# Kernel optimization log

Hardware: AMD Instinct MI355X
Metric: run time of the kernel (lower is better)

The kernel has to match this reference:

```python
import jax, jax.numpy as jnp
import numpy as np
from jax import lax

BS = 16; NG = 512; L = 2048; HOP = 512; ZD = 128; HD = 512
FS = L // 2 + 1
TAR = (NG - 1) * HOP + L  # 263680, matches int((NG+3)/4*L)
PPC = 5; PPK = 65
LOG10 = float(np.log(10.0))

def _hann_periodic(n):
    return (0.5 * (1.0 - np.cos(2.0 * np.pi * np.arange(n) / n))).astype(np.float32)

# filter window: fftshift(hann_window(L)) (torch periodic hann)
_FW = jnp.asarray(np.fft.fftshift(_hann_periodic(L)))
# OLA windows with edge correction (first/last grain half set to center value 1.0)
_w = _hann_periodic(L)
_ow = np.tile(_w[None, :], (NG, 1))
_ow[0, : L // 2] = _w[L // 2]
_ow[-1, L // 2 :] = _w[L // 2]
_OLA_W = jnp.asarray(_ow)  # [NG, L]
# overlap-add scatter indices and divisor (fold(unfold(ones)))
_IDX = jnp.asarray((np.arange(NG)[:, None] * HOP + np.arange(L)[None, :]).reshape(-1))
_DIV = jnp.zeros((TAR,), jnp.float32).at[_IDX].add(1.0)


def setup_inputs() -> dict:
    key = jax.random.key(0)
    ks = jax.random.split(key, 8)
    s = 0.02
    d = {}
    d["z"] = jax.random.normal(ks[0], (BS * NG, ZD), jnp.float32)
    d["w0"] = jax.random.normal(ks[1], (ZD, HD), jnp.float32) * s
    d["b0"] = jnp.zeros((HD,), jnp.float32)
    d["g0"] = jnp.ones((HD,), jnp.float32)
    d["be0"] = jnp.zeros((HD,), jnp.float32)
    d["w1"] = jax.random.normal(ks[2], (HD, HD), jnp.float32) * s
    d["b1"] = jnp.zeros((HD,), jnp.float32)
    d["g1"] = jnp.ones((HD,), jnp.float32)
    d["be1"] = jnp.zeros((HD,), jnp.float32)
    d["w2"] = jax.random.normal(ks[3], (HD, HD), jnp.float32) * s
    d["b2"] = jnp.zeros((HD,), jnp.float32)
    d["g2"] = jnp.ones((HD,), jnp.float32)
    d["be2"] = jnp.zeros((HD,), jnp.float32)
    d["w3"] = jax.random.normal(ks[4], (HD, FS), jnp.float32) * s
    d["b3"] = jnp.zeros((FS,), jnp.float32)
    d["pp_w"] = jax.random.normal(ks[5], (1, PPC, PPK), jnp.float32) * s
    d["pp_b"] = jnp.zeros((1,), jnp.float32)
    d["noise"] = jax.random.uniform(ks[6], (BS * NG, L), jnp.float32) * 2.0 - 1.0
    return d


def _lin_bn_lrelu(x, w, b, g, be):
    h = x @ w + b
    m = h.mean(0)
    v = jnp.mean((h - m) ** 2, 0)  # biased var (train-mode BatchNorm1d)
    h = (h - m) * lax.rsqrt(v + 1e-5) * g + be
    return jnp.where(h >= 0, h, 0.2 * h)  # LeakyReLU(0.2)


def reference(z, w0, b0, g0, be0, w1, b1, g1, be1, w2, b2, g2, be2, w3, b3, pp_w, pp_b, noise):
    # decoder MLP -> filter coefficients
    h = _lin_bn_lrelu(z, w0, b0, g0, be0)
    h = _lin_bn_lrelu(h, w1, b1, g1, be1)
    h = _lin_bn_lrelu(h, w2, b2, g2, be2)
    fc = h @ w3 + b3  # [BS*NG, FS]
    fc = 2.0 * jax.nn.sigmoid(fc) ** LOG10 + 1e-7  # mod_sigmoid
    # noise filtering in spectral domain
    ir = jnp.fft.irfft(fc.astype(jnp.complex64), n=L, axis=-1).astype(jnp.float32)
    ir = jnp.fft.fftshift(ir * _FW[None, :], axes=-1)
    audio = jnp.fft.irfft(jnp.fft.rfft(noise, axis=-1) * jnp.fft.rfft(ir, axis=-1), n=L, axis=-1).astype(jnp.float32)
    # per-grain windowing + overlap-add (nn.Fold equivalent scatter-add)
    audio = audio.reshape(BS, NG, L) * _OLA_W[None]
    audio_sum = jnp.zeros((BS, TAR), jnp.float32).at[:, _IDX].add(audio.reshape(BS, -1))
    audio_sum = audio_sum / _DIV  # normalize_ola
    # post-processing conv (PPC replicated channels -> 1) + softsign
    x = jnp.broadcast_to(audio_sum[:, None, :], (BS, PPC, TAR))
    y = lax.conv_general_dilated(x, pp_w, (1,), [(PPK // 2, PPK // 2)], dimension_numbers=("NCH", "OIH", "NCH"))
    y = y[:, 0, :] + pp_b[0]
    return y / (1.0 + jnp.abs(y))
```

## Files before the change

kernel.cpp:

```cpp
#include <hip/hip_runtime.h>
#include <hip/hip_bf16.h>
#include <math.h>

#define TARLEN 263680
#define POWEXP 2.302585092994046f
#define PC(i) ((i) + ((i) >> 3))

typedef __attribute__((ext_vector_type(8))) short bf16x8;
typedef __attribute__((ext_vector_type(8))) ushort u16x8;
typedef __attribute__((ext_vector_type(4))) float f32x4;

__device__ __forceinline__ void gload16(const void* g, void* l) {
    __builtin_amdgcn_global_load_lds((const __attribute__((address_space(1))) void*)g,
                                     (__attribute__((address_space(3))) void*)l, 16, 0, 0);
}

__device__ __forceinline__ float bf16f(ushort u) {
    union { uint u; float f; } v; v.u = (uint)u << 16; return v.f;
}
__device__ __forceinline__ ushort fbf16(float x) {
    __hip_bfloat16 h = __float2bfloat16(x);
    return *reinterpret_cast<ushort*>(&h);
}

__device__ __forceinline__ float vsin_rev(float rev) {
    float r; asm("v_sin_f32 %0, %1" : "=v"(r) : "v"(rev)); return r;
}
__device__ __forceinline__ float vcos_rev(float rev) {
    float r; asm("v_cos_f32 %0, %1" : "=v"(r) : "v"(rev)); return r;
}

template<int EPI>
__global__ __launch_bounds__(512) void gemm8(
    const ushort* __restrict__ A, const ushort* __restrict__ Bt,
    const float* __restrict__ bias, ushort* __restrict__ C,
    int K, int Nvalid, int ldc,
    float* __restrict__ ps, float* __restrict__ pq)
{
    __shared__ ushort As[3][4096];
    __shared__ ushort Bs[3][4096];
    __shared__ float sred[8][2][16];
    __shared__ float qred[8][2][16];
    const int tid = threadIdx.x;
    const int lane = tid & 63;
    const int wid = tid >> 6;
    const int nwg = gridDim.x * gridDim.y;
    const int bid = blockIdx.y * gridDim.x + blockIdx.x;
    const int q8 = nwg >> 3;
    const int swzb = (bid & 7) * q8 + (bid >> 3);
    const int bx = swzb % gridDim.x;
    const int by = swzb / gridDim.x;
    const int m0 = by * 128;
    const int n0 = bx * 128;
    const int NT = K >> 5;

    f32x4 acc[4][2];
#pragma unroll
    for (int m = 0; m < 4; ++m)
#pragma unroll
        for (int n = 0; n < 2; ++n)
            acc[m][n] = (f32x4){0.f, 0.f, 0.f, 0.f};

    const int srow = tid >> 2;
    const int scol = (((tid & 3) ^ ((tid >> 3) & 3)) << 3);

    auto stage = [&](int t, int buf) {
        const int k0 = t << 5;
        gload16(A + (size_t)(m0 + srow) * K + k0 + scol, &As[buf][tid * 8]);
        gload16(Bt + (size_t)(n0 + srow) * K + k0 + scol, &Bs[buf][tid * 8]);
    };

    const int lr = lane & 15;
    const int sw8 = (((lane >> 4) ^ ((lane >> 1) & 3)) << 3);
    const int wm0 = (wid >> 2) * 64;
    const int wn0 = (wid & 3) * 32;

    stage(0, 0);
    stage(1, 1);
    for (int t = 0; t < NT; ++t) {
        const int cur = t % 3;
        if (t + 2 < NT) {
            asm volatile("s_waitcnt vmcnt(2)" ::: "memory");
            __builtin_amdgcn_s_barrier();
            stage(t + 2, (t + 2) % 3);
        } else {
            asm volatile("s_waitcnt vmcnt(0)" ::: "memory");
            __builtin_amdgcn_s_barrier();
        }
        const ushort* as = As[cur];
        const ushort* bs = Bs[cur];
        bf16x8 af[4], bfv[2];
#pragma unroll
        for (int m = 0; m < 4; ++m)
            af[m] = *reinterpret_cast<const bf16x8*>(&as[(wm0 + m * 16 + lr) * 32 + sw8]);
#pragma unroll
        for (int n = 0; n < 2; ++n)
            bfv[n] = *reinterpret_cast<const bf16x8*>(&bs[(wn0 + n * 16 + lr) * 32 + sw8]);
#pragma unroll
        for (int m = 0; m < 4; ++m)
#pragma unroll
            for (int n = 0; n < 2; ++n)
                acc[m][n] = __builtin_amdgcn_mfma_f32_16x16x32_bf16(af[m], bfv[n], acc[m][n], 0, 0, 0);
    }
    __syncthreads();

    const int cr = (lane >> 4) << 2;
    const int cc = lane & 15;
    float sacc[2] = {0.f, 0.f}, qacc[2] = {0.f, 0.f};
#pragma unroll
    for (int m = 0; m < 4; ++m) {
#pragma unroll
        for (int n = 0; n < 2; ++n) {
            int gcol = n0 + wn0 + n * 16 + cc;
            if (EPI == 0 || gcol < Nvalid) {
                float bv = bias[gcol];
                int grow = m0 + wm0 + m * 16 + cr;
#pragma unroll
                for (int j = 0; j < 4; ++j) {
                    float v = acc[m][n][j] + bv;
                    if (EPI == 1) {
                        float sg = 1.f / (1.f + __expf(-v));
                        v = 2.f * __expf(POWEXP * __logf(sg)) + 1e-7f;
                    } else {
                        sacc[n] += v;
                        qacc[n] += v * v;
                    }
                    C[(size_t)(grow + j) * ldc + gcol] = fbf16(v);
                }
            }
        }
    }
    if (EPI == 0) {
#pragma unroll
        for (int n = 0; n < 2; ++n) {
            float s = sacc[n], q = qacc[n];
            s += __shfl_xor(s, 16); q += __shfl_xor(q, 16);
            s += __shfl_xor(s, 32); q += __shfl_xor(q, 32);
            if (lane < 16) { sred[wid][n][lane] = s; qred[wid][n][lane] = q; }
        }
        __syncthreads();
        if (tid < 128) {
            int wn_ = tid >> 5, n_ = (tid >> 4) & 1, cc_ = tid & 15;
            float s = sred[wn_][n_][cc_] + sred[4 + wn_][n_][cc_];
            float q = qred[wn_][n_][cc_] + qred[4 + wn_][n_][cc_];
            int col = n0 + wn_ * 32 + n_ * 16 + cc_;
            ps[(size_t)by * 512 + col] = s;
            pq[(size_t)by * 512 + col] = q;
        }
    }
}

__global__ __launch_bounds__(256) void prep_stats_act_k(
    const ushort* __restrict__ Hb, const float* __restrict__ ps,
    const float* __restrict__ pq, const float* __restrict__ gamma,
    const float* __restrict__ beta, ushort* __restrict__ A)
{
    __shared__ float sa[512], sb[512];
    const int tid = threadIdx.x;
    for (int c = tid; c < 512; c += 256) {
        float s = 0.f, q = 0.f;
#pragma unroll 8
        for (int rg = 0; rg < 64; ++rg) { s += ps[rg * 512 + c]; q += pq[rg * 512 + c]; }
        float m = s * (1.f / 8192.f);
        float v = q * (1.f / 8192.f) - m * m;
        float rs = rsqrtf(v + 1e-5f);
        float a = rs * gamma[c];
        sa[c] = a;
        sb[c] = beta[c] - m * a;
    }
    __syncthreads();
    const int col0 = (tid * 8) & 511;
    float ra[8], rb[8];
#pragma unroll
    for (int j = 0; j < 8; ++j) { ra[j] = sa[col0 + j]; rb[j] = sb[col0 + j]; }
    size_t base = (size_t)blockIdx.x * 16384;
#pragma unroll
    for (int it = 0; it < 8; ++it) {
        int off = (it * 256 + tid) << 3;
        u16x8 hv = *reinterpret_cast<const u16x8*>(&Hb[base + off]);
        u16x8 o;
#pragma unroll
        for (int j = 0; j < 8; ++j) {
            float y = fmaf(bf16f(hv[j]), ra[j], rb[j]);
            o[j] = fbf16(y >= 0.f ? y : 0.2f * y);
        }
        *reinterpret_cast<u16x8*>(&A[base + off]) = o;
    }
}

__global__ __launch_bounds__(256) void prep_inputs(
    const float* __restrict__ w0, const float* __restrict__ w1,
    const float* __restrict__ w2, const float* __restrict__ w3,
    const float* __restrict__ z,
    ushort* __restrict__ B0, ushort* __restrict__ B1,
    ushort* __restrict__ B2, ushort* __restrict__ B3,
    ushort* __restrict__ A)
{
    if (blockIdx.z == 4) {
        int bid = blockIdx.y * gridDim.x + blockIdx.x;
        if (bid >= 512) return;
        int idx = (bid * 256 + threadIdx.x) << 3;
        float4 a = *reinterpret_cast<const float4*>(&z[idx]);
        float4 b = *reinterpret_cast<const float4*>(&z[idx + 4]);
        float x[8] = {a.x, a.y, a.z, a.w, b.x, b.y, b.z, b.w};
        u16x8 o;
#pragma unroll
        for (int j = 0; j < 8; ++j) o[j] = fbf16(x[j]);
        *reinterpret_cast<u16x8*>(&A[idx]) = o;
        return;
    }
    const float* w; ushort* Bt; int K, N, GX, GY;
    switch (blockIdx.z) {
        case 0: w = w0; Bt = B0; K = 128; N = 512;  GX = 4;  GY = 16; break;
        case 1: w = w1; Bt = B1; K = 512; N = 512;  GX = 16; GY = 16; break;
        case 2: w = w2; Bt = B2; K = 512; N = 512;  GX = 16; GY = 16; break;
        default:w = w3; Bt = B3; K = 512; N = 1025; GX = 16; GY = 36; break;
    }
    if ((int)blockIdx.x >= GX || (int)blockIdx.y >= GY) return;
    __shared__ float tile[32][33];
    int k0 = blockIdx.x * 32, n0 = blockIdx.y * 32;
    int tx = threadIdx.x & 31, ty = threadIdx.x >> 5;
#pragma unroll
    for (int r = 0; r < 4; ++r) {
        int k = k0 + ty + r * 8;
        int n = n0 + tx;
        tile[ty + r * 8][tx] = (n < N) ? w[(size_t)k * N + n] : 0.f;
    }
    __syncthreads();
#pragma unroll
    for (int r = 0; r < 4; ++r) {
        int n = n0 + ty + r * 8;
        int k = k0 + tx;
        Bt[(size_t)n * K + k] = fbf16(tile[tx][ty + r * 8]);
    }
}

__device__ __forceinline__ float2 cmul(float2 a, float c, float s) {
    return make_float2(a.x * c - a.y * s, a.x * s + a.y * c);
}

template<bool INV, int L>
__device__ __forceinline__ void stk_stage(
    const float2* __restrict__ s, float2* __restrict__ d, int t)
{
    int k = t & (L - 1);
    float2 x0 = s[PC(t)];
    float2 x1 = s[PC(t + 256)];
    float2 x2 = s[PC(t + 512)];
    float2 x3 = s[PC(t + 768)];
    if (L > 1) {
        float rev = (float)k * (1.0f / (float)(4 * L));
        float s1 = vsin_rev(rev), c1 = vcos_rev(rev);
        if (!INV) s1 = -s1;
        float c2 = c1 * c1 - s1 * s1, s2 = 2.f * c1 * s1;
        float c3 = c2 * c1 - s2 * s1, s3 = s2 * c1 + c2 * s1;
        x1 = cmul(x1, c1, s1);
        x2 = cmul(x2, c2, s2);
        x3 = cmul(x3, c3, s3);
    }
    float2 a = make_float2(x0.x + x2.x, x0.y + x2.y);
    float2 b = make_float2(x0.x - x2.x, x0.y - x2.y);
    float2 c = make_float2(x1.x + x3.x, x1.y + x3.y);
    float2 e = make_float2(x1.x - x3.x, x1.y - x3.y);
    int db = ((t - k) << 2) + k;
    d[PC(db)]         = make_float2(a.x + c.x, a.y + c.y);
    d[PC(db + 2 * L)] = make_float2(a.x - c.x, a.y - c.y);
    if (!INV) {
        d[PC(db + L)]     = make_float2(b.x + e.y, b.y - e.x);
        d[PC(db + 3 * L)] = make_float2(b.x - e.y, b.y + e.x);
    } else {
        d[PC(db + L)]     = make_float2(b.x - e.y, b.y + e.x);
        d[PC(db + 3 * L)] = make_float2(b.x + e.y, b.y - e.x);
    }
}

__global__ __launch_bounds__(256) void fft_filter_kernel(
    const float* __restrict__ noise, const ushort* __restrict__ fcsb,
    ushort* __restrict__ awb)
{
    __shared__ float2 X[1152], Y[1152];
    __shared__ ushort Fb[1026];
    const int tid = threadIdx.x;
    const int r = blockIdx.x;

    const float2* nrow = reinterpret_cast<const float2*>(noise + ((size_t)r << 11));
    for (int i = tid; i < 1025; i += 256) Fb[i] = fcsb[(size_t)r * 1040 + i];
    {
        float2 x0 = nrow[tid], x1 = nrow[tid + 256], x2 = nrow[tid + 512], x3 = nrow[tid + 768];
        float2 a = make_float2(x0.x + x2.x, x0.y + x2.y);
        float2 b = make_float2(x0.x - x2.x, x0.y - x2.y);
        float2 c = make_float2(x1.x + x3.x, x1.y + x3.y);
        float2 e = make_float2(x1.x - x3.x, x1.y - x3.y);
        int db = tid << 2;
        Y[PC(db)]     = make_float2(a.x + c.x, a.y + c.y);
        Y[PC(db + 1)] = make_float2(b.x + e.y, b.y - e.x);
        Y[PC(db + 2)] = make_float2(a.x - c.x, a.y - c.y);
        Y[PC(db + 3)] = make_float2(b.x - e.y, b.y + e.x);
    }
    __syncthreads();
    stk_stage<false, 4>(Y, X, tid);   __syncthreads();
    stk_stage<false, 16>(X, Y, tid);  __syncthreads();
    stk_stage<false, 64>(Y, X, tid);  __syncthreads();
    stk_stage<false, 256>(X, Y, tid); __syncthreads();

    const float INV1024 = 1.0f / 1024.0f;
    auto proc = [&](int k, float c, float s) {
        int k2 = (1024 - k) & 1023;
        float2 za = Y[PC(k)], zb = Y[PC(k2)];
        float Fer = 0.5f * (za.x + zb.x), Fei = 0.5f * (za.y - zb.y);
        float For = 0.5f * (za.y + zb.y), Foi = 0.5f * (zb.x - za.x);
        float wFr = c * For - s * Foi;
        float wFi = c * Foi + s * For;
        float Xkr = Fer + wFr, Xki = Fei + wFi;
        float Xbr = Fer - wFr, Xbi = wFi - Fei;
        float Hk, Hb;
        {
            float cl = (k == 0) ? bf16f(Fb[1]) : bf16f(Fb[k - 1]);
            float crr = (k == 1024) ? bf16f(Fb[1023]) : bf16f(Fb[k + 1]);
            float h = 0.5f * bf16f(Fb[k]) + 0.25f * (cl + crr);
            Hk = ((k & 1) ? -h : h) * INV1024;
        }
        {
            int kb = 1024 - k;
            float cl = (kb == 0) ? bf16f(Fb[1]) : bf16f(Fb[kb - 1]);
            float crr = (kb == 1024) ? bf16f(Fb[1023]) : bf16f(Fb[kb + 1]);
            float h = 0.5f * bf16f(Fb[kb]) + 0.25f * (cl + crr);
            Hb = ((kb & 1) ? -h : h) * INV1024;
        }
        float Ykr = Hk * Xkr, Yki = Hk * Xki;
        float Ybr = Hb * Xbr, Ybi = Hb * Xbi;
        if (k == 0) {
            X[PC(0)] = make_float2(0.5f * (Ykr + Ybr), 0.5f * (Ykr - Ybr));
        } else {
            float Ger = 0.5f * (Ykr + Ybr), Gei = 0.5f * (Yki - Ybi);
            float Sgr = 0.5f * (Ykr - Ybr), Sgi = 0.5f * (Yki + Ybi);
            float wpr = c, wpi = -s;
            float Gor = wpr * Sgr - wpi * Sgi;
            float Goi = wpr * Sgi + wpi * Sgr;
            X[PC(k)]  = make_float2(Ger - Goi, Gei + Gor);
            X[PC(k2)] = make_float2(Ger + Goi, Gor - Gei);
        }
    };
    {
        float rev0 = (float)tid * (1.0f / 2048.0f);
        float c0 = vcos_rev(rev0), s0 = -vsin_rev(rev0);
        proc(tid, c0, s0);
        float rev1 = (float)(tid + 256) * (1.0f / 2048.0f);
        float c1 = vcos_rev(rev1), s1 = -vsin_rev(rev1);
        proc(tid + 256, c1, s1);
        if (tid == 0) proc(512, 0.f, -1.f);
    }
    __syncthreads();

    stk_stage<true, 1>(X, Y, tid);  __syncthreads();
    stk_stage<true, 4>(Y, X, tid);  __syncthreads();
    stk_stage<true, 16>(X, Y, tid); __syncthreads();
    stk_stage<true, 64>(Y, X, tid); __syncthreads();

    {
        const int g = r & 511;
        ushort2* awrow = reinterpret_cast<ushort2*>(awb + ((size_t)r << 11));
        int t = tid;
        float2 x0 = X[PC(t)], x1 = X[PC(t + 256)], x2 = X[PC(t + 512)], x3 = X[PC(t + 768)];
        float rev = (float)t * (1.0f / 1024.0f);
        float s1 = vsin_rev(rev), c1 = vcos_rev(rev);
        float c2 = c1 * c1 - s1 * s1, s2 = 2.f * c1 * s1;
        float c3 = c2 * c1 - s2 * s1, s3 = s2 * c1 + c2 * s1;
        x1 = cmul(x1, c1, s1);
        x2 = cmul(x2, c2, s2);
        x3 = cmul(x3, c3, s3);
        float2 a = make_float2(x0.x + x2.x, x0.y + x2.y);
        float2 b = make_float2(x0.x - x2.x, x0.y - x2.y);
        float2 c = make_float2(x1.x + x3.x, x1.y + x3.y);
        float2 e = make_float2(x1.x - x3.x, x1.y - x3.y);
        float2 o[4];
        o[0] = make_float2(a.x + c.x, a.y + c.y);
        o[1] = make_float2(b.x - e.y, b.y + e.x);
        o[2] = make_float2(a.x - c.x, a.y - c.y);
        o[3] = make_float2(b.x + e.y, b.y - e.x);
        float cq[4] = {c1, -s1, -c1, s1};
        float sq[4] = {s1, c1, -s1, -c1};
        const float COSD = 0.99999529380958f;
        const float SIND = 0.00306795676296f;
#pragma unroll
        for (int q = 0; q < 4; ++q) {
            int n = t + 256 * q;
            float w0, w1;
            bool edge = (g == 0 && q < 2) || (g == 511 && q >= 2);
            if (edge) { w0 = 1.f; w1 = 1.f; }
            else {
                w0 = 0.5f - 0.5f * cq[q];
                w1 = 0.5f - 0.5f * (cq[q] * COSD - sq[q] * SIND);
            }
            ushort2 ov; ov.x = fbf16(o[q].x * w0); ov.y = fbf16(o[q].y * w1);
            awrow[n] = ov;
        }
    }
}

__global__ __launch_bounds__(256) void ola_ppconv_kernel(
    const ushort* __restrict__ awb, const float* __restrict__ ppw,
    const float* __restrict__ ppb, float* __restrict__ out)
{
    __shared__ float tile[320];
    __shared__ float Ksh[65];
    int t0 = blockIdx.x * 256;
    int b = blockIdx.y;
    const ushort* awbase = awb + ((size_t)(b * 512) << 11);
    for (int i = threadIdx.x; i < 320; i += 256) {
        int tt = t0 - 32 + i;
        float v = 0.f;
        if (tt >= 1536 && tt < 262144) {
            int glo = (tt - 1536) >> 9;
            const ushort* p = awbase + ((size_t)glo << 11) + (tt - (glo << 9));
            float s = bf16f(p[0]) + bf16f(p[1536]) + bf16f(p[3072]) + bf16f(p[4608]);
            v = s * 0.25f;
        } else if (tt >= 0 && tt < TARLEN) {
            int ghi = min(511, tt >> 9);
            int glo = max(0, (tt - 1536) >> 9);
            float s = 0.f;
            for (int g = glo; g <= ghi; ++g) {
                int n = tt - (g << 9);
                s += bf16f(awbase[((size_t)g << 11) + n]);
            }
            v = s / (float)(ghi - glo + 1);
        }
        tile[i] = v;
    }
    if (threadIdx.x < 65) {
        float k = 0.f;
#pragma unroll
        for (int c = 0; c < 5; ++c) k += ppw[c * 65 + threadIdx.x];
        Ksh[threadIdx.x] = k;
    }
    __syncthreads();
    float y = ppb[0];
#pragma unroll
    for (int j = 0; j < 65; ++j) y = fmaf(Ksh[j], tile[threadIdx.x + j], y);
    int t = t0 + threadIdx.x;
    out[(size_t)b * TARLEN + t] = y / (1.f + fabsf(y));
}

extern "C" void kernel_launch(void* const* d_in, const int* in_sizes, int n_in,
                              void* d_out, int out_size, void* d_ws, size_t ws_size,
                              hipStream_t stream) {
    const float* z    = (const float*)d_in[0];
    const float* w0   = (const float*)d_in[1];
    const float* b0   = (const float*)d_in[2];
    const float* g0   = (const float*)d_in[3];
    const float* be0  = (const float*)d_in[4];
    const float* w1   = (const float*)d_in[5];
    const float* b1   = (const float*)d_in[6];
    const float* g1   = (const float*)d_in[7];
    const float* be1  = (const float*)d_in[8];
    const float* w2   = (const float*)d_in[9];
    const float* b2   = (const float*)d_in[10];
    const float* g2   = (const float*)d_in[11];
    const float* be2  = (const float*)d_in[12];
    const float* w3   = (const float*)d_in[13];
    const float* b3   = (const float*)d_in[14];
    const float* ppw  = (const float*)d_in[15];
    const float* ppb  = (const float*)d_in[16];
    const float* noise= (const float*)d_in[17];
    float* out = (float*)d_out;
    float* ws = (float*)d_ws;

    ushort* h0b = (ushort*)ws;
    ushort* h1b = (ushort*)(ws + 2097152);
    float* ps   = ws + 4194304;
    float* pq   = ps + 32768;
    float* base = pq + 32768 + 1024;
    ushort* Bt0 = (ushort*)base;
    ushort* Bt1 = (ushort*)(base + 32768);
    ushort* Bt2 = (ushort*)(base + 163840);
    ushort* Bt3 = (ushort*)(base + 294912);
    ushort* fcsb= (ushort*)(base + 589824);
    ushort* awb = (ushort*)(base + 589824 + 4259840);
    ushort* A   = (ushort*)(base + 589824 + 4259840 + 8388608);
    ushort* h2b = h0b;

    dim3 blk(256);
    dim3 gblk(512);
    prep_inputs<<<dim3(16, 36, 5), blk, 0, stream>>>(
        w0, w1, w2, w3, z, Bt0, Bt1, Bt2, Bt3, A);
    gemm8<0><<<dim3(4, 64), gblk, 0, stream>>>(A, Bt0, b0, h0b, 128, 512, 512, ps, pq);
    prep_stats_act_k<<<dim3(256), blk, 0, stream>>>(h0b, ps, pq, g0, be0, A);
    gemm8<0><<<dim3(4, 64), gblk, 0, stream>>>(A, Bt1, b1, h1b, 512, 512, 512, ps, pq);
    prep_stats_act_k<<<dim3(256), blk, 0, stream>>>(h1b, ps, pq, g1, be1, A);
    gemm8<0><<<dim3(4, 64), gblk, 0, stream>>>(A, Bt2, b2, h2b, 512, 512, 512, ps, pq);
    prep_stats_act_k<<<dim3(256), blk, 0, stream>>>(h2b, ps, pq, g2, be2, A);
    gemm8<1><<<dim3(9, 64), gblk, 0, stream>>>(A, Bt3, b3, fcsb, 512, 1025, 1040, nullptr, nullptr);
    fft_filter_kernel<<<dim3(8192), blk, 0, stream>>>(noise, fcsb, awb);
    ola_ppconv_kernel<<<dim3(1030, 16), blk, 0, stream>>>(awb, ppw, ppb, out);
    (void)in_sizes; (void)n_in; (void)out_size; (void)ws_size;
}
```

Baseline: 173.4 us.

## Fuse BatchNorm stats finalize and LeakyReLU into next GEMM's A-operand load

Removes the three separate prep_stats_act_k kernels by having each following GEMM reduce the partial column sums itself, build per-column scale/shift in LDS (packed as bf16 pairs), and apply the normalization and LeakyReLU while staging A tiles through registers into LDS. Ping-pong stat buffers are added so a layer can read the previous stats while writing new ones. This saves three launches and a full read/write pass of the 8192x512 activation. In exchange every GEMM block repeats the 64-row stat reduction, A now goes through registers instead of direct global-to-LDS loads, and scale/shift are rounded to bf16.

```diff
diff --git a/kernel.cpp b/kernel.cpp
--- a/kernel.cpp
+++ b/kernel.cpp
@@ -30,12 +30,10 @@
     float r; asm("v_cos_f32 %0, %1" : "=v"(r) : "v"(rev)); return r;
 }
 
-template<int EPI>
 __global__ __launch_bounds__(512) void gemm8(
     const ushort* __restrict__ A, const ushort* __restrict__ Bt,
     const float* __restrict__ bias, ushort* __restrict__ C,
-    int K, int Nvalid, int ldc,
-    float* __restrict__ ps, float* __restrict__ pq)
+    int K, float* __restrict__ ps, float* __restrict__ pq)
 {
     __shared__ ushort As[3][4096];
     __shared__ ushort Bs[3][4096];
@@ -112,6 +110,151 @@
 #pragma unroll
         for (int n = 0; n < 2; ++n) {
             int gcol = n0 + wn0 + n * 16 + cc;
+            float bv = bias[gcol];
+            int grow = m0 + wm0 + m * 16 + cr;
+#pragma unroll
+            for (int j = 0; j < 4; ++j) {
+                float v = acc[m][n][j] + bv;
+                sacc[n] += v;
+                qacc[n] += v * v;
+                C[(size_t)(grow + j) * 512 + gcol] = fbf16(v);
+            }
+        }
+    }
+#pragma unroll
+    for (int n = 0; n < 2; ++n) {
+        float s = sacc[n], q = qacc[n];
+        s += __shfl_xor(s, 16); q += __shfl_xor(q, 16);
+        s += __shfl_xor(s, 32); q += __shfl_xor(q, 32);
+        if (lane < 16) { sred[wid][n][lane] = s; qred[wid][n][lane] = q; }
+    }
+    __syncthreads();
+    if (tid < 128) {
+        int wn_ = tid >> 5, n_ = (tid >> 4) & 1, cc_ = tid & 15;
+        float s = sred[wn_][n_][cc_] + sred[4 + wn_][n_][cc_];
+        float q = qred[wn_][n_][cc_] + qred[4 + wn_][n_][cc_];
+        int col = n0 + wn_ * 32 + n_ * 16 + cc_;
+        ps[(size_t)by * 512 + col] = s;
+        pq[(size_t)by * 512 + col] = q;
+    }
+}
+
+template<int EPI>
+__global__ __launch_bounds__(512) void gemm8n(
+    const ushort* __restrict__ H, const ushort* __restrict__ Bt,
+    const float* __restrict__ bias,
+    const float* __restrict__ psIn, const float* __restrict__ pqIn,
+    const float* __restrict__ gamma, const float* __restrict__ beta,
+    ushort* __restrict__ C, int K, int Nvalid, int ldc,
+    float* __restrict__ psOut, float* __restrict__ pqOut)
+{
+    __shared__ ushort As[3][4096];
+    __shared__ ushort Bs[3][4096];
+    __shared__ uint sab[512];
+    __shared__ float sred[8][2][16];
+    __shared__ float qred[8][2][16];
+    const int tid = threadIdx.x;
+    const int lane = tid & 63;
+    const int wid = tid >> 6;
+    const int nwg = gridDim.x * gridDim.y;
+    const int bid = blockIdx.y * gridDim.x + blockIdx.x;
+    const int q8 = nwg >> 3;
+    const int swzb = (bid & 7) * q8 + (bid >> 3);
+    const int bx = swzb % gridDim.x;
+    const int by = swzb / gridDim.x;
+    const int m0 = by * 128;
+    const int n0 = bx * 128;
+    const int NT = K >> 5;
+
+    {
+        int c = tid;
+        float s = 0.f, q = 0.f;
+#pragma unroll 8
+        for (int rg = 0; rg < 64; ++rg) { s += psIn[rg * 512 + c]; q += pqIn[rg * 512 + c]; }
+        float m = s * (1.f / 8192.f);
+        float v = q * (1.f / 8192.f) - m * m;
+        float a = rsqrtf(v + 1e-5f) * gamma[c];
+        float b = beta[c] - m * a;
+        sab[c] = (uint)fbf16(a) | ((uint)fbf16(b) << 16);
+    }
+
+    f32x4 acc[4][2];
+#pragma unroll
+    for (int m = 0; m < 4; ++m)
+#pragma unroll
+        for (int n = 0; n < 2; ++n)
+            acc[m][n] = (f32x4){0.f, 0.f, 0.f, 0.f};
+
+    const int srow = tid >> 2;
+    const int scol = (((tid & 3) ^ ((tid >> 3) & 3)) << 3);
+    const int lr = lane & 15;
+    const int sw8 = (((lane >> 4) ^ ((lane >> 1) & 3)) << 3);
+    const int wm0 = (wid >> 2) * 64;
+    const int wn0 = (wid & 3) * 32;
+
+    const size_t arow = (size_t)(m0 + srow) * K + scol;
+    const size_t brow = (size_t)(n0 + srow) * K + scol;
+
+    auto stageB = [&](int t, int buf) {
+        gload16(Bt + brow + (t << 5), &Bs[buf][tid * 8]);
+    };
+    auto loadA = [&](int t, u16x8& dst) {
+        dst = *reinterpret_cast<const u16x8*>(H + arow + (t << 5));
+    };
+
+    __syncthreads();
+
+    u16x8 a0, a1;
+    stageB(0, 0); loadA(0, a0);
+    stageB(1, 1); loadA(1, a1);
+
+    auto iter = [&](int t, u16x8& ar) {
+        const int cur = t % 3;
+        if (t + 2 < NT) asm volatile("s_waitcnt vmcnt(2)" ::: "memory");
+        else            asm volatile("s_waitcnt vmcnt(0)" ::: "memory");
+        {
+            const uint* pk = &sab[(t << 5) + scol];
+            u16x8 o;
+#pragma unroll
+            for (int j = 0; j < 8; ++j) {
+                uint w = pk[j];
+                float a = bf16f((ushort)(w & 0xffffu));
+                float b = bf16f((ushort)(w >> 16));
+                float y = fmaf(bf16f(ar[j]), a, b);
+                o[j] = fbf16(y >= 0.f ? y : 0.2f * y);
+            }
+            *reinterpret_cast<u16x8*>(&As[cur][tid * 8]) = o;
+        }
+        asm volatile("s_waitcnt lgkmcnt(0)" ::: "memory");
+        __builtin_amdgcn_s_barrier();
+        if (t + 2 < NT) { stageB(t + 2, (t + 2) % 3); loadA(t + 2, ar); }
+        const ushort* as = As[cur];
+        const ushort* bs = Bs[cur];
+        bf16x8 af[4], bfv[2];
+#pragma unroll
+        for (int m = 0; m < 4; ++m)
+            af[m] = *reinterpret_cast<const bf16x8*>(&as[(wm0 + m * 16 + lr) * 32 + sw8]);
+#pragma unroll
+        for (int n = 0; n < 2; ++n)
+            bfv[n] = *reinterpret_cast<const bf16x8*>(&bs[(wn0 + n * 16 + lr) * 32 + sw8]);
+#pragma unroll
+        for (int m = 0; m < 4; ++m)
+#pragma unroll
+            for (int n = 0; n < 2; ++n)
+                acc[m][n] = __builtin_amdgcn_mfma_f32_16x16x32_bf16(af[m], bfv[n], acc[m][n], 0, 0, 0);
+    };
+
+    for (int t = 0; t < NT; t += 2) { iter(t, a0); iter(t + 1, a1); }
+    __syncthreads();
+
+    const int cr = (lane >> 4) << 2;
+    const int cc = lane & 15;
+    float sacc[2] = {0.f, 0.f}, qacc[2] = {0.f, 0.f};
+#pragma unroll
+    for (int m = 0; m < 4; ++m) {
+#pragma unroll
+        for (int n = 0; n < 2; ++n) {
+            int gcol = n0 + wn0 + n * 16 + cc;
             if (EPI == 0 || gcol < Nvalid) {
                 float bv = bias[gcol];
                 int grow = m0 + wm0 + m * 16 + cr;
@@ -144,47 +287,9 @@
             float s = sred[wn_][n_][cc_] + sred[4 + wn_][n_][cc_];
             float q = qred[wn_][n_][cc_] + qred[4 + wn_][n_][cc_];
             int col = n0 + wn_ * 32 + n_ * 16 + cc_;
-            ps[(size_t)by * 512 + col] = s;
-            pq[(size_t)by * 512 + col] = q;
-        }
-    }
-}
-
-__global__ __launch_bounds__(256) void prep_stats_act_k(
-    const ushort* __restrict__ Hb, const float* __restrict__ ps,
-    const float* __restrict__ pq, const float* __restrict__ gamma,
-    const float* __restrict__ beta, ushort* __restrict__ A)
-{
-    __shared__ float sa[512], sb[512];
-    const int tid = threadIdx.x;
-    for (int c = tid; c < 512; c += 256) {
-        float s = 0.f, q = 0.f;
-#pragma unroll 8
-        for (int rg = 0; rg < 64; ++rg) { s += ps[rg * 512 + c]; q += pq[rg * 512 + c]; }
-        float m = s * (1.f / 8192.f);
-        float v = q * (1.f / 8192.f) - m * m;
-        float rs = rsqrtf(v + 1e-5f);
-        float a = rs * gamma[c];
-        sa[c] = a;
-        sb[c] = beta[c] - m * a;
-    }
-    __syncthreads();
-    const int col0 = (tid * 8) & 511;
-    float ra[8], rb[8];
-#pragma unroll
-    for (int j = 0; j < 8; ++j) { ra[j] = sa[col0 + j]; rb[j] = sb[col0 + j]; }
-    size_t base = (size_t)blockIdx.x * 16384;
-#pragma unroll
-    for (int it = 0; it < 8; ++it) {
-        int off = (it * 256 + tid) << 3;
-        u16x8 hv = *reinterpret_cast<const u16x8*>(&Hb[base + off]);
-        u16x8 o;
-#pragma unroll
-        for (int j = 0; j < 8; ++j) {
-            float y = fmaf(bf16f(hv[j]), ra[j], rb[j]);
-            o[j] = fbf16(y >= 0.f ? y : 0.2f * y);
-        }
-        *reinterpret_cast<u16x8*>(&A[base + off]) = o;
+            psOut[(size_t)by * 512 + col] = s;
+            pqOut[(size_t)by * 512 + col] = q;
+        }
     }
 }
 
@@ -467,29 +572,31 @@
 
     ushort* h0b = (ushort*)ws;
     ushort* h1b = (ushort*)(ws + 2097152);
-    float* ps   = ws + 4194304;
-    float* pq   = ps + 32768;
-    float* base = pq + 32768 + 1024;
+    float* ps0  = ws + 4194304;
+    float* pq0  = ps0 + 32768;
+    float* ps1  = pq0 + 32768;
+    float* pq1  = ps1 + 32768;
+    float* base = pq1 + 32768;
     ushort* Bt0 = (ushort*)base;
     ushort* Bt1 = (ushort*)(base + 32768);
     ushort* Bt2 = (ushort*)(base + 163840);
     ushort* Bt3 = (ushort*)(base + 294912);
     ushort* fcsb= (ushort*)(base + 589824);
-    ushort* awb = (ushort*)(base + 589824 + 4259840);
-    ushort* A   = (ushort*)(base + 589824 + 4259840 + 8388608);
+    ushort* awb = (ushort*)(base + 4849664);
+    ushort* A   = (ushort*)(base + 13238272);
     ushort* h2b = h0b;
 
     dim3 blk(256);
     dim3 gblk(512);
     prep_inputs<<<dim3(16, 36, 5), blk, 0, stream>>>(
         w0, w1, w2, w3, z, Bt0, Bt1, Bt2, Bt3, A);
-    gemm8<0><<<dim3(4, 64), gblk, 0, stream>>>(A, Bt0, b0, h0b, 128, 512, 512, ps, pq);
-    prep_stats_act_k<<<dim3(256), blk, 0, stream>>>(h0b, ps, pq, g0, be0, A);
-    gemm8<0><<<dim3(4, 64), gblk, 0, stream>>>(A, Bt1, b1, h1b, 512, 512, 512, ps, pq);
-    prep_stats_act_k<<<dim3(256), blk, 0, stream>>>(h1b, ps, pq, g1, be1, A);
-    gemm8<0><<<dim3(4, 64), gblk, 0, stream>>>(A, Bt2, b2, h2b, 512, 512, 512, ps, pq);
-    prep_stats_act_k<<<dim3(256), blk, 0, stream>>>(h2b, ps, pq, g2, be2, A);
-    gemm8<1><<<dim3(9, 64), gblk, 0, stream>>>(A, Bt3, b3, fcsb, 512, 1025, 1040, nullptr, nullptr);
+    gemm8<<<dim3(4, 64), gblk, 0, stream>>>(A, Bt0, b0, h0b, 128, ps0, pq0);
+    gemm8n<0><<<dim3(4, 64), gblk, 0, stream>>>(
+        h0b, Bt1, b1, ps0, pq0, g0, be0, h1b, 512, 512, 512, ps1, pq1);
+    gemm8n<0><<<dim3(4, 64), gblk, 0, stream>>>(
+        h1b, Bt2, b2, ps1, pq1, g1, be1, h2b, 512, 512, 512, ps0, pq0);
+    gemm8n<1><<<dim3(9, 64), gblk, 0, stream>>>(
+        h2b, Bt3, b3, ps0, pq0, g2, be2, fcsb, 512, 1025, 1040, nullptr, nullptr);
     fft_filter_kernel<<<dim3(8192), blk, 0, stream>>>(noise, fcsb, awb);
     ola_ppconv_kernel<<<dim3(1030, 16), blk, 0, stream>>>(awb, ppw, ppb, out);
     (void)in_sizes; (void)n_in; (void)out_size; (void)ws_size;
```

After: 162.2 us. -6.5%, faster.
